# Kernel tuning notes

Measured on AMD Instinct MI355X. Metric: run time of the kernel, lower is better.

## Reference

```python
import jax, jax.numpy as jnp
import numpy as np

B = 16384
F = 26          # num categorical fields
V = 100000      # vocab per field (equal sizes)
N = 13          # num numeric fields
D = 32          # embed_dim
HIDDEN = [256, 128, 64]


def setup_inputs() -> dict:
    key = jax.random.key(0)
    ks = jax.random.split(key, 16)
    x_cat = jax.random.randint(ks[0], (B, F), 0, V)
    x_num = jax.random.normal(ks[1], (B, N), dtype=jnp.float32)
    # first-order and second-order embedding tables (all fields stacked)
    emb0 = jax.random.normal(ks[2], (F, V), dtype=jnp.float32) * 0.01      # linear weights per cat value
    emb1 = jax.random.normal(ks[3], (F, V, D), dtype=jnp.float32) * 0.01   # latent vectors per cat value
    num_bias = jnp.zeros((N,), dtype=jnp.float32)
    num_emb = jax.random.normal(ks[4], (N, D), dtype=jnp.float32) * 0.01
    # MLP params: input_dim = (F+N)*D -> 256 -> 128 -> 64
    dims = [(F + N) * D] + HIDDEN
    params = {}
    for i in range(len(HIDDEN)):
        fan_in = dims[i]
        bound = 1.0 / np.sqrt(fan_in)
        params[f"W{i+1}"] = jax.random.uniform(ks[5 + 2 * i], (fan_in, dims[i + 1]), minval=-bound, maxval=bound, dtype=jnp.float32)
        params[f"b{i+1}"] = jax.random.uniform(ks[6 + 2 * i], (dims[i + 1],), minval=-bound, maxval=bound, dtype=jnp.float32)
    head_in = HIDDEN[-1] + 2
    hb = 1.0 / np.sqrt(head_in)
    Wc = jax.random.uniform(ks[11], (head_in, 1), minval=-hb, maxval=hb, dtype=jnp.float32)
    bc = jax.random.uniform(ks[12], (1,), minval=-hb, maxval=hb, dtype=jnp.float32)
    Wo = jax.random.uniform(ks[13], (head_in, 1), minval=-hb, maxval=hb, dtype=jnp.float32)
    bo = jax.random.uniform(ks[14], (1,), minval=-hb, maxval=hb, dtype=jnp.float32)
    return {"x_cat": x_cat, "x_num": x_num, "emb0": emb0, "emb1": emb1,
            "num_bias": num_bias, "num_emb": num_emb,
            "W1": params["W1"], "b1": params["b1"],
            "W2": params["W2"], "b2": params["b2"],
            "W3": params["W3"], "b3": params["b3"],
            "Wc": Wc, "bc": bc, "Wo": Wo, "bo": bo}


def reference(x_cat, x_num, emb0, emb1, num_bias, num_emb,
              W1, b1, W2, b2, W3, b3, Wc, bc, Wo, bo):
    f_idx = jnp.arange(F)
    # ---- first-order (linear) term ----
    linear_cat = emb0[f_idx[None, :], x_cat]                 # [B, F]
    linear_num = x_num * num_bias[None, :]                   # [B, N]
    linear_term = (linear_cat.sum(axis=1) + linear_num.sum(axis=1))[:, None]  # [B, 1]
    # ---- embeddings for FM + deep ----
    cat_e = emb1[f_idx[None, :], x_cat]                      # [B, F, D] fused gather
    num_e = x_num[:, :, None] * num_emb[None, :, :]          # [B, N, D]
    all_emb = jnp.concatenate([cat_e, num_e], axis=1)        # [B, F+N, D]
    # ---- FM second-order: 0.5 * sum((sum v)^2 - sum v^2) ----
    sum_emb = all_emb.sum(axis=1)                            # [B, D]
    square_sum = (all_emb * all_emb).sum(axis=1)             # [B, D]
    fm_second = 0.5 * (sum_emb * sum_emb - square_sum).sum(axis=1, keepdims=True)  # [B, 1]
    # ---- deep MLP (dropout = identity in eval) ----
    h = all_emb.reshape(all_emb.shape[0], -1)                # [B, (F+N)*D]
    h = jax.nn.relu(h @ W1 + b1)
    h = jax.nn.relu(h @ W2 + b2)
    h = jax.nn.relu(h @ W3 + b3)
    concat = jnp.concatenate([h, linear_term, fm_second], axis=1)  # [B, 66]
    logit1 = concat @ Wc + bc
    logit2 = concat @ Wo + bo
    return logit1, logit2
```

## Files before the change

### kernel.cpp

```cpp
#include <hip/hip_runtime.h>
#include <stdint.h>

#define B_ROWS 16384
#define NF 26
#define NV 100000
#define NN 13
#define ND 32
#define K1DIM 1248
#define H1DIM 256
#define H2DIM 128
#define H3DIM 64

typedef float f32x4 __attribute__((ext_vector_type(4)));
typedef short bf16x8 __attribute__((ext_vector_type(8)));

static __device__ __forceinline__ unsigned short f2bf(float f) {
    unsigned int u = __float_as_uint(f);
    unsigned int r = (u + 0x7fffu + ((u >> 16) & 1u)) >> 16;
    return (unsigned short)r;
}

#define S1P ((K1DIM/32)*H1DIM*32)
#define S2P ((H1DIM/32)*H2DIM*32)
#define S3P ((H2DIM/32)*H3DIM*32)

__global__ __launch_bounds__(256) void repack_weights(
    const float* __restrict__ W1, const float* __restrict__ W2, const float* __restrict__ W3,
    unsigned short* __restrict__ W1p, unsigned short* __restrict__ W2p, unsigned short* __restrict__ W3p)
{
    int tid = blockIdx.x * 256 + threadIdx.x;
    if (tid < S1P) {
        int kk = tid & 31; int n = (tid >> 5) & (H1DIM - 1); int kt = tid >> 13;
        W1p[tid] = f2bf(W1[(kt * 32 + kk) * H1DIM + n]);
    } else if (tid < S1P + S2P) {
        int t = tid - S1P;
        int kk = t & 31; int n = (t >> 5) & (H2DIM - 1); int kt = t >> 12;
        W2p[t] = f2bf(W2[(kt * 32 + kk) * H2DIM + n]);
    } else if (tid < S1P + S2P + S3P) {
        int t = tid - S1P - S2P;
        int kk = t & 31; int n = (t >> 5) & (H3DIM - 1); int kt = t >> 11;
        W3p[t] = f2bf(W3[(kt * 32 + kk) * H3DIM + n]);
    }
}

__global__ __launch_bounds__(256) void embed_fm(
    const int* __restrict__ x_cat, const float* __restrict__ x_num,
    const float* __restrict__ emb0, const float* __restrict__ emb1,
    const float* __restrict__ num_bias, const float* __restrict__ num_emb,
    unsigned short* __restrict__ Xp, float* __restrict__ lin_out, float* __restrict__ fm_out)
{
    int grp = threadIdx.x >> 5;
    int d   = threadIdx.x & 31;
    int row = blockIdx.x * 8 + grp;

    const int* xc = x_cat + row * NF;
    int   myidx = (d < NF) ? xc[d] : 0;
    float xn    = (d < NN) ? x_num[row * NN + d] : 0.f;

    float lv = 0.f;
    if (d < NF) lv = emb0[d * NV + myidx];
    if (d < NN) lv += xn * num_bias[d];

    unsigned short* xr = Xp + (size_t)row * K1DIM;
    float s = 0.f, q = 0.f;
#pragma unroll
    for (int f = 0; f < NF; ++f) {
        int idx = __shfl(myidx, f, 32);
        float e = emb1[((size_t)(f * NV + idx)) * ND + d];
        s += e; q += e * e;
        xr[f * ND + d] = f2bf(e);
    }
#pragma unroll
    for (int n = 0; n < NN; ++n) {
        float xv = __shfl(xn, n, 32);
        float e = xv * num_emb[n * ND + d];
        s += e; q += e * e;
        xr[(NF + n) * ND + d] = f2bf(e);
    }
    float val = s * s - q;
#pragma unroll
    for (int m = 16; m >= 1; m >>= 1) {
        val += __shfl_xor(val, m, 32);
        lv  += __shfl_xor(lv,  m, 32);
    }
    if (d == 0) { fm_out[row] = 0.5f * val; lin_out[row] = lv; }
}

template<int TMM, int TMN>
__global__ __launch_bounds__(256) void gemm_relu(
    const unsigned short* __restrict__ X, const unsigned short* __restrict__ Wp,
    const float* __restrict__ bias, unsigned short* __restrict__ Y,
    int M, int N, int K)
{
    int wave = blockIdx.x * 4 + (threadIdx.x >> 6);
    int lane = threadIdx.x & 63;
    int l15 = lane & 15, quad = lane >> 4;
    int nWaveN = N / (16 * TMN);
    int wm = wave / nWaveN, wn = wave % nWaveN;
    int m0 = wm * 16 * TMM, n0 = wn * 16 * TMN;

    f32x4 acc[TMM][TMN];
#pragma unroll
    for (int i = 0; i < TMM; i++)
#pragma unroll
        for (int j = 0; j < TMN; j++) acc[i][j] = (f32x4){0.f, 0.f, 0.f, 0.f};

    const unsigned short* aptr = X + (size_t)(m0 + l15) * K + quad * 8;
    const unsigned short* bptr = Wp + ((size_t)n0 + l15) * 32 + quad * 8;
    const int KT = K >> 5;

    bf16x8 a[TMM], b[TMN];
#pragma unroll
    for (int i = 0; i < TMM; i++) a[i] = *(const bf16x8*)(aptr + (size_t)i * 16 * K);
#pragma unroll
    for (int j = 0; j < TMN; j++) b[j] = *(const bf16x8*)(bptr + (size_t)j * 16 * 32);

    for (int kt = 0; kt < KT - 1; ++kt) {
        bf16x8 an[TMM], bn[TMN];
        const unsigned short* ap = aptr + (size_t)(kt + 1) * 32;
        const unsigned short* bp = bptr + (size_t)(kt + 1) * N * 32;
#pragma unroll
        for (int i = 0; i < TMM; i++) an[i] = *(const bf16x8*)(ap + (size_t)i * 16 * K);
#pragma unroll
        for (int j = 0; j < TMN; j++) bn[j] = *(const bf16x8*)(bp + (size_t)j * 16 * 32);
#pragma unroll
        for (int i = 0; i < TMM; i++)
#pragma unroll
            for (int j = 0; j < TMN; j++)
                acc[i][j] = __builtin_amdgcn_mfma_f32_16x16x32_bf16(a[i], b[j], acc[i][j], 0, 0, 0);
#pragma unroll
        for (int i = 0; i < TMM; i++) a[i] = an[i];
#pragma unroll
        for (int j = 0; j < TMN; j++) b[j] = bn[j];
    }
#pragma unroll
    for (int i = 0; i < TMM; i++)
#pragma unroll
        for (int j = 0; j < TMN; j++)
            acc[i][j] = __builtin_amdgcn_mfma_f32_16x16x32_bf16(a[i], b[j], acc[i][j], 0, 0, 0);

#pragma unroll
    for (int j = 0; j < TMN; j++) {
        int col = n0 + j * 16 + l15;
        float bv = bias[col];
#pragma unroll
        for (int i = 0; i < TMM; i++) {
            int rbase = m0 + i * 16 + quad * 4;
#pragma unroll
            for (int r = 0; r < 4; r++) {
                float v = acc[i][j][r] + bv;
                v = v > 0.f ? v : 0.f;
                Y[(size_t)(rbase + r) * N + col] = f2bf(v);
            }
        }
    }
}

#define LDP 136
__global__ __launch_bounds__(256) void gemm23_head(
    const unsigned short* __restrict__ H1, const unsigned short* __restrict__ W2p,
    const float* __restrict__ b2,
    const unsigned short* __restrict__ W3p, const float* __restrict__ b3,
    const float* __restrict__ Wc, const float* __restrict__ bc,
    const float* __restrict__ Wo, const float* __restrict__ bo,
    const float* __restrict__ lin, const float* __restrict__ fm,
    float* __restrict__ out)
{
    __shared__ unsigned short lds[4 * 16 * LDP];
    int wid  = threadIdx.x >> 6;
    int wave = blockIdx.x * 4 + wid;
    int lane = threadIdx.x & 63;
    int l15 = lane & 15, quad = lane >> 4;
    int m0 = wave * 16;
    unsigned short* wlds = lds + wid * 16 * LDP;

    f32x4 acc2[8];
#pragma unroll
    for (int j = 0; j < 8; j++) acc2[j] = (f32x4){0.f, 0.f, 0.f, 0.f};

    const unsigned short* aptr = H1 + (size_t)(m0 + l15) * H1DIM + quad * 8;
    const unsigned short* bptr = W2p + l15 * 32 + quad * 8;
#pragma unroll
    for (int kt = 0; kt < 8; ++kt) {
        bf16x8 a = *(const bf16x8*)(aptr + kt * 32);
#pragma unroll
        for (int j = 0; j < 8; j++) {
            bf16x8 b = *(const bf16x8*)(bptr + (kt * H2DIM + j * 16) * 32);
            acc2[j] = __builtin_amdgcn_mfma_f32_16x16x32_bf16(a, b, acc2[j], 0, 0, 0);
        }
    }
#pragma unroll
    for (int j = 0; j < 8; j++) {
        int col = j * 16 + l15;
        float bv = b2[col];
#pragma unroll
        for (int r = 0; r < 4; r++) {
            float v = acc2[j][r] + bv;
            v = v > 0.f ? v : 0.f;
            wlds[(quad * 4 + r) * LDP + col] = f2bf(v);
        }
    }
    __syncthreads();

    f32x4 acc3[4];
#pragma unroll
    for (int j = 0; j < 4; j++) acc3[j] = (f32x4){0.f, 0.f, 0.f, 0.f};

    const unsigned short* b3ptr = W3p + l15 * 32 + quad * 8;
#pragma unroll
    for (int kt = 0; kt < 4; ++kt) {
        bf16x8 a = *(const bf16x8*)(wlds + l15 * LDP + kt * 32 + quad * 8);
#pragma unroll
        for (int j = 0; j < 4; j++) {
            bf16x8 b = *(const bf16x8*)(b3ptr + (kt * H3DIM + j * 16) * 32);
            acc3[j] = __builtin_amdgcn_mfma_f32_16x16x32_bf16(a, b, acc3[j], 0, 0, 0);
        }
    }

    float s1r[4] = {0.f, 0.f, 0.f, 0.f};
    float s2r[4] = {0.f, 0.f, 0.f, 0.f};
#pragma unroll
    for (int j = 0; j < 4; j++) {
        int col = j * 16 + l15;
        float bv = b3[col], wc = Wc[col], wo = Wo[col];
#pragma unroll
        for (int r = 0; r < 4; r++) {
            float v = acc3[j][r] + bv;
            v = v > 0.f ? v : 0.f;
            s1r[r] += v * wc;
            s2r[r] += v * wo;
        }
    }
#pragma unroll
    for (int r = 0; r < 4; r++) {
#pragma unroll
        for (int m = 8; m >= 1; m >>= 1) {
            s1r[r] += __shfl_xor(s1r[r], m, 16);
            s2r[r] += __shfl_xor(s2r[r], m, 16);
        }
    }
    if (l15 == 0) {
        float wc64 = Wc[64], wc65 = Wc[65], wo64 = Wo[64], wo65 = Wo[65];
        float bcv = bc[0], bov = bo[0];
#pragma unroll
        for (int r = 0; r < 4; r++) {
            int row = m0 + quad * 4 + r;
            float lt = lin[row], f2 = fm[row];
            out[row]          = s1r[r] + lt * wc64 + f2 * wc65 + bcv;
            out[B_ROWS + row] = s2r[r] + lt * wo64 + f2 * wo65 + bov;
        }
    }
}

#define OFF_XP   ((size_t)0)
#define OFF_W1P  ((size_t)40894464)
#define OFF_W2P  (OFF_W1P + 638976)
#define OFF_W3P  (OFF_W2P + 65536)
#define OFF_H1   (OFF_W3P + 16384)
#define OFF_LIN  (OFF_H1 + 8388608)
#define OFF_FM   (OFF_LIN + 65536)

extern "C" void kernel_launch(void* const* d_in, const int* in_sizes, int n_in,
                              void* d_out, int out_size, void* d_ws, size_t ws_size,
                              hipStream_t stream)
{
    const int*   x_cat    = (const int*)d_in[0];
    const float* x_num    = (const float*)d_in[1];
    const float* emb0     = (const float*)d_in[2];
    const float* emb1     = (const float*)d_in[3];
    const float* num_bias = (const float*)d_in[4];
    const float* num_emb  = (const float*)d_in[5];
    const float* W1 = (const float*)d_in[6];
    const float* b1 = (const float*)d_in[7];
    const float* W2 = (const float*)d_in[8];
    const float* b2 = (const float*)d_in[9];
    const float* W3 = (const float*)d_in[10];
    const float* b3 = (const float*)d_in[11];
    const float* Wc = (const float*)d_in[12];
    const float* bc = (const float*)d_in[13];
    const float* Wo = (const float*)d_in[14];
    const float* bo = (const float*)d_in[15];
    float* out = (float*)d_out;

    char* ws = (char*)d_ws;
    unsigned short* Xp  = (unsigned short*)(ws + OFF_XP);
    unsigned short* W1p = (unsigned short*)(ws + OFF_W1P);
    unsigned short* W2p = (unsigned short*)(ws + OFF_W2P);
    unsigned short* W3p = (unsigned short*)(ws + OFF_W3P);
    unsigned short* H1  = (unsigned short*)(ws + OFF_H1);
    float* lin = (float*)(ws + OFF_LIN);
    float* fm  = (float*)(ws + OFF_FM);

    repack_weights<<<(S1P + S2P + S3P) / 256, 256, 0, stream>>>(W1, W2, W3, W1p, W2p, W3p);
    embed_fm<<<B_ROWS / 8, 256, 0, stream>>>(x_cat, x_num, emb0, emb1, num_bias, num_emb, Xp, lin, fm);
    gemm_relu<4, 2><<<512, 256, 0, stream>>>(Xp, W1p, b1, H1, B_ROWS, H1DIM, K1DIM);
    gemm23_head<<<B_ROWS / 16 / 4, 256, 0, stream>>>(H1, W2p, b2, W3p, b3, Wc, bc, Wo, bo, lin, fm, out);
}
```

Measured before the change: 458.5 us.

## Fuse weight repack into embedding kernel, vectorize gathers, retile first GEMM

Merges the weight-repack and embedding/FM kernels into one launch, with extra blocks handling the repack, so the two independent jobs can run concurrently and one launch is saved. The embedding path now uses 8 threads per row, each loading float4 slices of the 32-wide embedding vector, and packs the bf16 stores into 8-byte writes, giving wider memory transactions for the random gathers. The first GEMM is retiled from 4x2 to 2x2 MFMA tiles per wave with twice the blocks, trading per-wave reuse for more parallelism.

```diff
diff --git a/kernel.cpp b/kernel.cpp
--- a/kernel.cpp
+++ b/kernel.cpp
@@ -20,70 +20,90 @@
     return (unsigned short)r;
 }
 
+static __device__ __forceinline__ void store_bf4(unsigned short* p, f32x4 e) {
+    uint2 u;
+    u.x = (unsigned)f2bf(e.x) | ((unsigned)f2bf(e.y) << 16);
+    u.y = (unsigned)f2bf(e.z) | ((unsigned)f2bf(e.w) << 16);
+    *(uint2*)p = u;
+}
+
 #define S1P ((K1DIM/32)*H1DIM*32)
 #define S2P ((H1DIM/32)*H2DIM*32)
 #define S3P ((H2DIM/32)*H3DIM*32)
-
-__global__ __launch_bounds__(256) void repack_weights(
-    const float* __restrict__ W1, const float* __restrict__ W2, const float* __restrict__ W3,
-    unsigned short* __restrict__ W1p, unsigned short* __restrict__ W2p, unsigned short* __restrict__ W3p)
-{
-    int tid = blockIdx.x * 256 + threadIdx.x;
-    if (tid < S1P) {
-        int kk = tid & 31; int n = (tid >> 5) & (H1DIM - 1); int kt = tid >> 13;
-        W1p[tid] = f2bf(W1[(kt * 32 + kk) * H1DIM + n]);
-    } else if (tid < S1P + S2P) {
-        int t = tid - S1P;
-        int kk = t & 31; int n = (t >> 5) & (H2DIM - 1); int kt = t >> 12;
-        W2p[t] = f2bf(W2[(kt * 32 + kk) * H2DIM + n]);
-    } else if (tid < S1P + S2P + S3P) {
-        int t = tid - S1P - S2P;
-        int kk = t & 31; int n = (t >> 5) & (H3DIM - 1); int kt = t >> 11;
-        W3p[t] = f2bf(W3[(kt * 32 + kk) * H3DIM + n]);
-    }
-}
-
-__global__ __launch_bounds__(256) void embed_fm(
+#define EMB_BLOCKS 512
+#define RPK_BLOCKS ((S1P + S2P + S3P) / 256)
+
+__global__ __launch_bounds__(256) void prep(
     const int* __restrict__ x_cat, const float* __restrict__ x_num,
     const float* __restrict__ emb0, const float* __restrict__ emb1,
     const float* __restrict__ num_bias, const float* __restrict__ num_emb,
-    unsigned short* __restrict__ Xp, float* __restrict__ lin_out, float* __restrict__ fm_out)
+    const float* __restrict__ W1, const float* __restrict__ W2, const float* __restrict__ W3,
+    unsigned short* __restrict__ Xp, float* __restrict__ lin_out, float* __restrict__ fm_out,
+    unsigned short* __restrict__ W1p, unsigned short* __restrict__ W2p, unsigned short* __restrict__ W3p)
 {
-    int grp = threadIdx.x >> 5;
-    int d   = threadIdx.x & 31;
-    int row = blockIdx.x * 8 + grp;
+    if (blockIdx.x >= EMB_BLOCKS) {
+        int tid = (blockIdx.x - EMB_BLOCKS) * 256 + threadIdx.x;
+        if (tid < S1P) {
+            int kk = tid & 31; int n = (tid >> 5) & (H1DIM - 1); int kt = tid >> 13;
+            W1p[tid] = f2bf(W1[(kt * 32 + kk) * H1DIM + n]);
+        } else if (tid < S1P + S2P) {
+            int t = tid - S1P;
+            int kk = t & 31; int n = (t >> 5) & (H2DIM - 1); int kt = t >> 12;
+            W2p[t] = f2bf(W2[(kt * 32 + kk) * H2DIM + n]);
+        } else {
+            int t = tid - S1P - S2P;
+            int kk = t & 31; int n = (t >> 5) & (H3DIM - 1); int kt = t >> 11;
+            W3p[t] = f2bf(W3[(kt * 32 + kk) * H3DIM + n]);
+        }
+        return;
+    }
+
+    int sub = threadIdx.x & 7;
+    int row = blockIdx.x * 32 + (threadIdx.x >> 3);
+    int lanebase = (threadIdx.x & 63) & 56;
 
     const int* xc = x_cat + row * NF;
-    int   myidx = (d < NF) ? xc[d] : 0;
-    float xn    = (d < NN) ? x_num[row * NN + d] : 0.f;
+    int idxh[4];
+#pragma unroll
+    for (int j = 0; j < 4; j++) { int f = sub + 8 * j; idxh[j] = (f < NF) ? xc[f] : 0; }
+    float numh[2];
+    numh[0] = x_num[row * NN + sub];
+    numh[1] = (sub < NN - 8) ? x_num[row * NN + sub + 8] : 0.f;
 
     float lv = 0.f;
-    if (d < NF) lv = emb0[d * NV + myidx];
-    if (d < NN) lv += xn * num_bias[d];
+#pragma unroll
+    for (int j = 0; j < 4; j++) { int f = sub + 8 * j; if (f < NF) lv += emb0[f * NV + idxh[j]]; }
+    lv += numh[0] * num_bias[sub];
+    if (sub < NN - 8) lv += numh[1] * num_bias[sub + 8];
 
     unsigned short* xr = Xp + (size_t)row * K1DIM;
-    float s = 0.f, q = 0.f;
+    f32x4 s4 = (f32x4){0.f, 0.f, 0.f, 0.f};
+    f32x4 q4 = (f32x4){0.f, 0.f, 0.f, 0.f};
+
 #pragma unroll
     for (int f = 0; f < NF; ++f) {
-        int idx = __shfl(myidx, f, 32);
-        float e = emb1[((size_t)(f * NV + idx)) * ND + d];
-        s += e; q += e * e;
-        xr[f * ND + d] = f2bf(e);
+        int idx = __shfl(idxh[f >> 3], lanebase + (f & 7), 64);
+        f32x4 e = ((const f32x4*)(emb1 + (size_t)(f * NV + idx) * ND))[sub];
+        s4 += e; q4 += e * e;
+        store_bf4(xr + f * ND + sub * 4, e);
     }
 #pragma unroll
     for (int n = 0; n < NN; ++n) {
-        float xv = __shfl(xn, n, 32);
-        float e = xv * num_emb[n * ND + d];
-        s += e; q += e * e;
-        xr[(NF + n) * ND + d] = f2bf(e);
-    }
-    float val = s * s - q;
-#pragma unroll
-    for (int m = 16; m >= 1; m >>= 1) {
-        val += __shfl_xor(val, m, 32);
-        lv  += __shfl_xor(lv,  m, 32);
-    }
-    if (d == 0) { fm_out[row] = 0.5f * val; lin_out[row] = lv; }
+        float xv = __shfl(numh[n >> 3], lanebase + (n & 7), 64);
+        f32x4 w = ((const f32x4*)(num_emb + n * ND))[sub];
+        f32x4 e = w * xv;
+        s4 += e; q4 += e * e;
+        store_bf4(xr + (NF + n) * ND + sub * 4, e);
+    }
+
+    float val = s4.x * s4.x + s4.y * s4.y + s4.z * s4.z + s4.w * s4.w
+              - (q4.x + q4.y + q4.z + q4.w);
+#pragma unroll
+    for (int m = 1; m < 8; m <<= 1) {
+        val += __shfl_xor(val, m, 64);
+        lv  += __shfl_xor(lv,  m, 64);
+    }
+    if (sub == 0) { fm_out[row] = 0.5f * val; lin_out[row] = lv; }
 }
 
 template<int TMM, int TMN>
@@ -291,8 +311,9 @@
     float* lin = (float*)(ws + OFF_LIN);
     float* fm  = (float*)(ws + OFF_FM);
 
-    repack_weights<<<(S1P + S2P + S3P) / 256, 256, 0, stream>>>(W1, W2, W3, W1p, W2p, W3p);
-    embed_fm<<<B_ROWS / 8, 256, 0, stream>>>(x_cat, x_num, emb0, emb1, num_bias, num_emb, Xp, lin, fm);
-    gemm_relu<4, 2><<<512, 256, 0, stream>>>(Xp, W1p, b1, H1, B_ROWS, H1DIM, K1DIM);
+    prep<<<EMB_BLOCKS + RPK_BLOCKS, 256, 0, stream>>>(
+        x_cat, x_num, emb0, emb1, num_bias, num_emb, W1, W2, W3,
+        Xp, lin, fm, W1p, W2p, W3p);
+    gemm_relu<2, 2><<<1024, 256, 0, stream>>>(Xp, W1p, b1, H1, B_ROWS, H1DIM, K1DIM);
     gemm23_head<<<B_ROWS / 16 / 4, 256, 0, stream>>>(H1, W2p, b2, W3p, b3, Wc, bc, Wo, bo, lin, fm, out);
 }
```

New measurement: 466.6 us. About the same (+1.8%).
